# Kernel optimization log

Measured on AMD Instinct MI355X. Metric: run time of the kernel, lower is better.

## Reference

```python
import jax, jax.numpy as jnp
import numpy as np

N_NODES = 100000
N_EDGES = 1000000
IN_CH, HID_CH, N_CLS = 128, 64, 40


def setup_inputs() -> dict:
    key = jax.random.key(0)
    ks = jax.random.split(key, 8)
    x = jax.random.normal(ks[0], (N_NODES, IN_CH), dtype=jnp.float32)
    edge_index = jax.random.randint(ks[1], (2, N_EDGES), 0, N_NODES, dtype=jnp.int32)
    # Glorot-ish scaled weights (ARMAConv init_weight / root_weight, K=1 stack squeezed)
    w1_init = jax.random.normal(ks[2], (IN_CH, HID_CH), dtype=jnp.float32) / np.sqrt(IN_CH)
    w1_root = jax.random.normal(ks[3], (IN_CH, HID_CH), dtype=jnp.float32) / np.sqrt(IN_CH)
    b1 = jnp.zeros((HID_CH,), dtype=jnp.float32)
    w2_init = jax.random.normal(ks[4], (HID_CH, N_CLS), dtype=jnp.float32) / np.sqrt(HID_CH)
    w2_root = jax.random.normal(ks[5], (HID_CH, N_CLS), dtype=jnp.float32) / np.sqrt(HID_CH)
    b2 = jnp.zeros((N_CLS,), dtype=jnp.float32)
    return {"x": x, "edge_index": edge_index,
            "w1_init": w1_init, "w1_root": w1_root, "b1": b1,
            "w2_init": w2_init, "w2_root": w2_root, "b2": b2}


def _arma_layer(x, row, col, norm, w_init, w_root, bias):
    # ARMAConv, num_stacks=1, num_layers=1, shared_weights=True, eval mode (dropout=id):
    # out = relu( A_hat @ (x W_init) + x W_root + b ), mean over the single stack.
    h = x @ w_init                           # [N, F_out]
    msg = norm[:, None] * h[row]             # gather from source nodes, [E, F_out]
    agg = jax.ops.segment_sum(msg, col, num_segments=N_NODES)  # scatter-add at targets
    return jax.nn.relu(agg + x @ w_root + bias)


def reference(x, edge_index, w1_init, w1_root, b1, w2_init, w2_root, b2):
    row, col = edge_index[0], edge_index[1]
    # gcn_norm, add_self_loops=False: deg over targets, norm = d^-1/2[row] * d^-1/2[col]
    deg = jax.ops.segment_sum(jnp.ones((row.shape[0],), x.dtype), col, num_segments=N_NODES)
    dinv = jnp.where(deg > 0, jax.lax.rsqrt(jnp.maximum(deg, 1e-12)), jnp.zeros_like(deg))
    norm = dinv[row] * dinv[col]
    h = _arma_layer(x, row, col, norm, w1_init, w1_root, b1)
    h = jax.nn.relu(h)  # BiARMA relu; dropout identity in eval
    return _arma_layer(h, row, col, norm, w2_init, w2_root, b2)
```

## Files before the change

kernel.cpp:

```cpp
#include <hip/hip_runtime.h>

#define N_NODES 100000
#define N_EDGES 1000000
#define IN_CH 128
#define HID_CH 64
#define N_CLS 40

#define NBUCK 782
#define GEMM_GRID 1024

static inline int cdiv(int a, int b) { return (a + b - 1) / b; }

using bf16x8 = __attribute__((ext_vector_type(8))) short;
using f32x4  = __attribute__((ext_vector_type(4))) float;

__device__ __forceinline__ unsigned pack_bf2(float a, float b) {
    unsigned ua = __float_as_uint(a), ub = __float_as_uint(b);
    ua += 0x7fffu + ((ua >> 16) & 1u);
    ub += 0x7fffu + ((ub >> 16) & 1u);
    return (ua >> 16) | (ub & 0xffff0000u);
}
__device__ __forceinline__ unsigned short bf16_of(float a) {
    unsigned ua = __float_as_uint(a);
    ua += 0x7fffu + ((ua >> 16) & 1u);
    return (unsigned short)(ua >> 16);
}
__device__ __forceinline__ float bf_lo(unsigned u) { return __uint_as_float(u << 16); }
__device__ __forceinline__ float bf_hi(unsigned u) { return __uint_as_float(u & 0xffff0000u); }


__global__ __launch_bounds__(256)
void bucket_count_kernel(const int* __restrict__ cols, int* __restrict__ gcount, int E) {
    __shared__ int hist[NBUCK];
    for (int i = threadIdx.x; i < NBUCK; i += 256) hist[i] = 0;
    __syncthreads();
    int per = (E + gridDim.x - 1) / gridDim.x;
    int s = blockIdx.x * per;
    int e = min(E, s + per);
    for (int j = s + threadIdx.x; j < e; j += 256)
        atomicAdd(&hist[cols[j] >> 7], 1);
    __syncthreads();
    for (int i = threadIdx.x; i < NBUCK; i += 256)
        if (hist[i]) atomicAdd(&gcount[i], hist[i]);
}


__global__ __launch_bounds__(1024)
void scan_bucket_kernel(const int* __restrict__ gcount, int* __restrict__ boff,
                        int* __restrict__ gcursor, int* __restrict__ offsets) {
    __shared__ int part[1024];
    int t = threadIdx.x;
    part[t] = (t < NBUCK) ? gcount[t] : 0;
    __syncthreads();
    for (int off = 1; off < 1024; off <<= 1) {
        int v = (t >= off) ? part[t - off] : 0;
        __syncthreads();
        part[t] += v;
        __syncthreads();
    }
    int excl = (t > 0) ? part[t - 1] : 0;
    if (t < NBUCK) { boff[t] = excl; gcursor[t] = excl; }
    if (t == NBUCK) { boff[NBUCK] = excl; offsets[N_NODES] = excl; }
}


__global__ __launch_bounds__(256)
void bucket_scatter_kernel(const int* __restrict__ rows, const int* __restrict__ cols,
                           int* __restrict__ gcursor, int* __restrict__ pedge, int E) {
    __shared__ int cur[NBUCK];
    for (int i = threadIdx.x; i < NBUCK; i += 256) cur[i] = 0;
    __syncthreads();
    int per = (E + gridDim.x - 1) / gridDim.x;
    int s = blockIdx.x * per;
    int e = min(E, s + per);
    for (int j = s + threadIdx.x; j < e; j += 256)
        atomicAdd(&cur[cols[j] >> 7], 1);
    __syncthreads();
    for (int i = threadIdx.x; i < NBUCK; i += 256) {
        int h = cur[i];
        cur[i] = h ? atomicAdd(&gcursor[i], h) : 0;
    }
    __syncthreads();
    for (int j = s + threadIdx.x; j < e; j += 256) {
        int c = cols[j];
        int pos = atomicAdd(&cur[c >> 7], 1);
        pedge[pos] = (rows[j] << 7) | (c & 127);
    }
}


__global__ __launch_bounds__(256)
void bucket_sort_kernel(const int* __restrict__ boff, const int* __restrict__ pedge,
                        int* __restrict__ srow, int* __restrict__ offsets,
                        float* __restrict__ dinv) {
    __shared__ int cnt[128];
    __shared__ int scn[128];
    __shared__ int cur[128];
    int b = blockIdx.x, t = threadIdx.x;
    if (t < 128) cnt[t] = 0;
    __syncthreads();
    int e0 = boff[b], e1 = boff[b + 1];
    for (int j = e0 + t; j < e1; j += 256)
        atomicAdd(&cnt[pedge[j] & 127], 1);
    __syncthreads();
    if (t < 128) scn[t] = cnt[t];
    __syncthreads();
    for (int off = 1; off < 128; off <<= 1) {
        int v = 0;
        if (t < 128 && t >= off) v = scn[t - off];
        __syncthreads();
        if (t < 128) scn[t] += v;
        __syncthreads();
    }
    if (t < 128) {
        int excl = (t > 0) ? scn[t - 1] : 0;
        cur[t] = excl;
        int node = b * 128 + t;
        if (node < N_NODES) {
            offsets[node] = e0 + excl;
            dinv[node] = cnt[t] ? rsqrtf((float)cnt[t]) : 0.f;
        }
    }
    __syncthreads();
    for (int j = e0 + t; j < e1; j += 256) {
        int p = pedge[j];
        int pos = atomicAdd(&cur[p & 127], 1);
        srow[e0 + pos] = p >> 7;
    }
}


__global__ __launch_bounds__(256)
void wconv_kernel(const float* __restrict__ w1i, const float* __restrict__ w1r,
                  const float* __restrict__ w2i, const float* __restrict__ w2r,
                  unsigned* __restrict__ wtgA, unsigned* __restrict__ wtgB) {
    int id = blockIdx.x * 256 + threadIdx.x;
    if (id < 128 * 64) {
        int c = id >> 6, kp = id & 63;
        int k = kp * 2;
        const float* W = (c < 64) ? w1i : w1r;
        int cc = (c < 64) ? c : c - 64;
        float a = W[(size_t)k * 64 + cc];
        float b = W[(size_t)(k + 1) * 64 + cc];
        wtgA[c * 64 + kp] = pack_bf2(a, b);
    } else if (id < 128 * 64 + 80 * 32) {
        int j = id - 128 * 64;
        int c = j >> 5, kp = j & 31;
        int k = kp * 2;
        const float* W = (c < 40) ? w2i : w2r;
        int cc = (c < 40) ? c : c - 40;
        float a = W[(size_t)k * 40 + cc];
        float b = W[(size_t)(k + 1) * 40 + cc];
        wtgB[c * 32 + kp] = pack_bf2(a, b);
    }
}


template<int K, int C1, int C2>
__launch_bounds__(256, 4)
__global__ void gemm_persist_kernel(const float* __restrict__ X,
                                    const unsigned short* __restrict__ WT,
                                    const float* __restrict__ Bias,
                                    const float* __restrict__ dinv,
                                    unsigned short* __restrict__ Y1b,
                                    float* __restrict__ Y2, int N, int ntiles) {
    constexpr int CT = C1 + C2;
    constexpr int NT = CT / 16;
    constexpr int KS = K / 32;
    constexpr int KP = K / 2 + 4;
    static_assert(CT % 16 == 0 && K % 32 == 0, "shape");

    __shared__ unsigned wt[CT * KP];

    const int tid = threadIdx.x;
    const int wave = tid >> 6;
    const int lane = tid & 63;
    const int m = lane & 15;
    const int quad = lane >> 4;

    constexpr int WDW = CT * (K / 2);
    const unsigned* wtg = (const unsigned*)WT;
    for (int i = tid * 4; i < WDW; i += 256 * 4) {
        int c = i / (K / 2);
        int j = i - c * (K / 2);
        uint4 v = *reinterpret_cast<const uint4*>(wtg + i);
        *reinterpret_cast<uint4*>(&wt[c * KP + j]) = v;
    }
    __syncthreads();

    float biasv[NT];
#pragma unroll
    for (int t = 0; t < NT; ++t) {
        int c = t * 16 + m;
        biasv[t] = (c >= C1) ? Bias[c - C1] : 0.f;
    }

    for (int tile = blockIdx.x; tile < ntiles; tile += gridDim.x) {
        const int rowA = tile * 64 + wave * 16 + m;
        const bool va = (rowA < N);
        const float* xr = X + (size_t)rowA * K + quad * 8;

        union AFrag { uint4 u; bf16x8 v; } af[KS];
#pragma unroll
        for (int ks = 0; ks < KS; ++ks) {
            float4 v0 = make_float4(0.f, 0.f, 0.f, 0.f);
            float4 v1 = make_float4(0.f, 0.f, 0.f, 0.f);
            if (va) {
                v0 = *reinterpret_cast<const float4*>(xr + ks * 32);
                v1 = *reinterpret_cast<const float4*>(xr + ks * 32 + 4);
            }
            af[ks].u.x = pack_bf2(v0.x, v0.y);
            af[ks].u.y = pack_bf2(v0.z, v0.w);
            af[ks].u.z = pack_bf2(v1.x, v1.y);
            af[ks].u.w = pack_bf2(v1.z, v1.w);
        }

        f32x4 acc[NT];
#pragma unroll
        for (int t = 0; t < NT; ++t) acc[t] = (f32x4){0.f, 0.f, 0.f, 0.f};
#pragma unroll
        for (int ks = 0; ks < KS; ++ks) {
#pragma unroll
            for (int t = 0; t < NT; ++t) {
                bf16x8 b = *reinterpret_cast<const bf16x8*>(&wt[(t * 16 + m) * KP + ks * 16 + quad * 4]);
                acc[t] = __builtin_amdgcn_mfma_f32_16x16x32_bf16(af[ks].v, b, acc[t], 0, 0, 0);
            }
        }

        const int rbase = tile * 64 + wave * 16 + quad * 4;
        float dv[4];
#pragma unroll
        for (int reg = 0; reg < 4; ++reg)
            dv[reg] = (rbase + reg < N) ? dinv[rbase + reg] : 0.f;

#pragma unroll
        for (int t = 0; t < NT; ++t) {
            int c = t * 16 + m;
#pragma unroll
            for (int reg = 0; reg < 4; ++reg) {
                int r = rbase + reg;
                if (r >= N) continue;
                float v = acc[t][reg];
                if (c < C1) {
                    Y1b[(size_t)r * C1 + c] = bf16_of(v * dv[reg]);
                } else {
                    Y2[(size_t)r * C2 + (c - C1)] = v + biasv[t];
                }
            }
        }
    }
}


template<int K, int C1, int C2>
__launch_bounds__(256)
__global__ void gemm_mfma_fused_kernel(const float* __restrict__ X,
                                       const float* __restrict__ W1,
                                       const float* __restrict__ W2,
                                       const float* __restrict__ Bias,
                                       const float* __restrict__ dinv,
                                       unsigned short* __restrict__ Y1b,
                                       float* __restrict__ Y2, int N) {
    constexpr int CT = C1 + C2;
    constexpr int NT = CT / 16;
    constexpr int KS = K / 32;
    constexpr int KP = (K + 8) / 2;
    static_assert(CT % 16 == 0 && K % 32 == 0, "shape");
    static_assert(C1 % 4 == 0 && C2 % 4 == 0, "staging vec4");

    __shared__ unsigned xb[64 * KP];
    __shared__ unsigned wt[CT * KP];
    __shared__ float dloc[64];

    const int tid = threadIdx.x;
    const int wave = tid >> 6;
    const int lane = tid & 63;
    const int m = lane & 15;
    const int quad = lane >> 4;
    const int r0 = blockIdx.x * 64;

    if (tid < 64) {
        int gr = r0 + tid;
        dloc[tid] = (gr < N) ? dinv[gr] : 0.f;
    }

    constexpr int XIT = 64 * (K / 4);
    for (int i = tid; i < XIT; i += 256) {
        int rr = i / (K / 4);
        int k4 = i - rr * (K / 4);
        int gr = r0 + rr;
        float4 v = make_float4(0.f, 0.f, 0.f, 0.f);
        if (gr < N)
            v = *reinterpret_cast<const float4*>(&X[(size_t)gr * K + k4 * 4]);
        uint2 p;
        p.x = pack_bf2(v.x, v.y);
        p.y = pack_bf2(v.z, v.w);
        *reinterpret_cast<uint2*>(&xb[rr * KP + k4 * 2]) = p;
    }

    constexpr int WIT = (K / 2) * (CT / 4);
    for (int i = tid; i < WIT; i += 256) {
        int kp = i / (CT / 4);
        int c4 = i - kp * (CT / 4);
        int k = kp * 2;
        int c = c4 * 4;
        float4 va, vb;
        if (c < C1) {
            va = *reinterpret_cast<const float4*>(&W1[(size_t)k * C1 + c]);
            vb = *reinterpret_cast<const float4*>(&W1[(size_t)(k + 1) * C1 + c]);
        } else {
            va = *reinterpret_cast<const float4*>(&W2[(size_t)k * C2 + (c - C1)]);
            vb = *reinterpret_cast<const float4*>(&W2[(size_t)(k + 1) * C2 + (c - C1)]);
        }
        wt[(c + 0) * KP + kp] = pack_bf2(va.x, vb.x);
        wt[(c + 1) * KP + kp] = pack_bf2(va.y, vb.y);
        wt[(c + 2) * KP + kp] = pack_bf2(va.z, vb.z);
        wt[(c + 3) * KP + kp] = pack_bf2(va.w, vb.w);
    }
    __syncthreads();

    const int rowbase = wave * 16;
    f32x4 acc[NT];
#pragma unroll
    for (int t = 0; t < NT; ++t) acc[t] = (f32x4){0.f, 0.f, 0.f, 0.f};

#pragma unroll
    for (int ks = 0; ks < KS; ++ks) {
        bf16x8 a = *reinterpret_cast<const bf16x8*>(&xb[(rowbase + m) * KP + ks * 16 + quad * 4]);
#pragma unroll
        for (int t = 0; t < NT; ++t) {
            bf16x8 b = *reinterpret_cast<const bf16x8*>(&wt[(t * 16 + m) * KP + ks * 16 + quad * 4]);
            acc[t] = __builtin_amdgcn_mfma_f32_16x16x32_bf16(a, b, acc[t], 0, 0, 0);
        }
    }

#pragma unroll
    for (int t = 0; t < NT; ++t) {
        int c = t * 16 + m;
        float bias = (c >= C1) ? Bias[c - C1] : 0.f;
#pragma unroll
        for (int reg = 0; reg < 4; ++reg) {
            int rl = rowbase + quad * 4 + reg;
            int r = r0 + rl;
            if (r >= N) continue;
            float v = acc[t][reg];
            if (c < C1) {
                Y1b[(size_t)r * C1 + c] = bf16_of(v * dloc[rl]);
            } else {
                Y2[(size_t)r * C2 + (c - C1)] = v + bias;
            }
        }
    }
}


template<int C>
__launch_bounds__(256)
__global__ void pull_bf16_kernel(const int* __restrict__ offsets,
                                 const int* __restrict__ srow,
                                 const float* __restrict__ dinv,
                                 const unsigned* __restrict__ H,
                                 float* __restrict__ Y, int N) {
    constexpr int TPE = C / 4;
    constexpr int CH = C / 2;
    int gid = blockIdx.x * blockDim.x + threadIdx.x;
    int node = gid / TPE;
    int lane = gid - node * TPE;
    if (node >= N) return;

    int e0 = offsets[node];
    int e1 = offsets[node + 1];
    float dc = dinv[node];

    float4 acc = make_float4(0.f, 0.f, 0.f, 0.f);
    int j = e0;
    for (; j + 4 <= e1; j += 4) {
        int r0 = srow[j + 0];
        int r1 = srow[j + 1];
        int r2 = srow[j + 2];
        int r3 = srow[j + 3];
        uint2 u0 = *reinterpret_cast<const uint2*>(&H[(size_t)r0 * CH + lane * 2]);
        uint2 u1 = *reinterpret_cast<const uint2*>(&H[(size_t)r1 * CH + lane * 2]);
        uint2 u2 = *reinterpret_cast<const uint2*>(&H[(size_t)r2 * CH + lane * 2]);
        uint2 u3 = *reinterpret_cast<const uint2*>(&H[(size_t)r3 * CH + lane * 2]);
        acc.x += (bf_lo(u0.x) + bf_lo(u1.x)) + (bf_lo(u2.x) + bf_lo(u3.x));
        acc.y += (bf_hi(u0.x) + bf_hi(u1.x)) + (bf_hi(u2.x) + bf_hi(u3.x));
        acc.z += (bf_lo(u0.y) + bf_lo(u1.y)) + (bf_lo(u2.y) + bf_lo(u3.y));
        acc.w += (bf_hi(u0.y) + bf_hi(u1.y)) + (bf_hi(u2.y) + bf_hi(u3.y));
    }
    for (; j < e1; ++j) {
        int r = srow[j];
        uint2 u = *reinterpret_cast<const uint2*>(&H[(size_t)r * CH + lane * 2]);
        acc.x += bf_lo(u.x);
        acc.y += bf_hi(u.x);
        acc.z += bf_lo(u.y);
        acc.w += bf_hi(u.y);
    }

    float4* Y4 = reinterpret_cast<float4*>(Y);
    size_t yi = (size_t)node * TPE + lane;
    float4 y = Y4[yi];
    y.x = fmaxf(fmaf(dc, acc.x, y.x), 0.f);
    y.y = fmaxf(fmaf(dc, acc.y, y.y), 0.f);
    y.z = fmaxf(fmaf(dc, acc.z, y.z), 0.f);
    y.w = fmaxf(fmaf(dc, acc.w, y.w), 0.f);
    Y4[yi] = y;
}


extern "C" void kernel_launch(void* const* d_in, const int* in_sizes, int n_in,
                              void* d_out, int out_size, void* d_ws, size_t ws_size,
                              hipStream_t stream) {
    const float* x       = (const float*)d_in[0];
    const int*   eidx    = (const int*)d_in[1];
    const float* w1_init = (const float*)d_in[2];
    const float* w1_root = (const float*)d_in[3];
    const float* b1      = (const float*)d_in[4];
    const float* w2_init = (const float*)d_in[5];
    const float* w2_root = (const float*)d_in[6];
    const float* b2      = (const float*)d_in[7];
    float* out = (float*)d_out;

    const int* rows = eidx;
    const int* cols = eidx + N_EDGES;

    int* wsi = (int*)d_ws;
    int*      gcount  = wsi;
    int*      boff    = wsi + 784;
    int*      gcursor = wsi + 1572;
    float*    dinv    = (float*)(wsi + 2360);
    int*      offsets = wsi + 102360;
    int*      srow    = wsi + 202364;
    unsigned* h0b     = (unsigned*)(wsi + 1202364);
    int*      pedge   = wsi + 1202364;
    float*    agg1    = (float*)(wsi + 4402364);
    unsigned* h2b     = h0b;
    unsigned* wtgA    = (unsigned*)(wsi + 10802364);
    unsigned* wtgB    = wtgA + 8192;
    const size_t WS_NEEDED = 10813116ull * 4ull;

    hipMemsetAsync(gcount, 0, 784 * sizeof(int), stream);
    bucket_count_kernel<<<128, 256, 0, stream>>>(cols, gcount, N_EDGES);
    scan_bucket_kernel<<<1, 1024, 0, stream>>>(gcount, boff, gcursor, offsets);
    bucket_scatter_kernel<<<128, 256, 0, stream>>>(rows, cols, gcursor, pedge, N_EDGES);
    bucket_sort_kernel<<<NBUCK, 256, 0, stream>>>(boff, pedge, srow, offsets, dinv);

    const int NTILES = cdiv(N_NODES, 64);

    if (ws_size >= WS_NEEDED) {
        wconv_kernel<<<42, 256, 0, stream>>>(w1_init, w1_root, w2_init, w2_root, wtgA, wtgB);

        gemm_persist_kernel<IN_CH, HID_CH, HID_CH><<<GEMM_GRID, 256, 0, stream>>>(
            x, (const unsigned short*)wtgA, b1, dinv, (unsigned short*)h0b, agg1,
            N_NODES, NTILES);
        pull_bf16_kernel<HID_CH><<<cdiv(N_NODES * (HID_CH / 4), 256), 256, 0, stream>>>(
            offsets, srow, dinv, h0b, agg1, N_NODES);

        gemm_persist_kernel<HID_CH, N_CLS, N_CLS><<<GEMM_GRID, 256, 0, stream>>>(
            agg1, (const unsigned short*)wtgB, b2, dinv, (unsigned short*)h2b, out,
            N_NODES, NTILES);
        pull_bf16_kernel<N_CLS><<<cdiv(N_NODES * (N_CLS / 4), 256), 256, 0, stream>>>(
            offsets, srow, dinv, h2b, out, N_NODES);
    } else {
        gemm_mfma_fused_kernel<IN_CH, HID_CH, HID_CH><<<NTILES, 256, 0, stream>>>(
            x, w1_init, w1_root, b1, dinv, (unsigned short*)h0b, agg1, N_NODES);
        pull_bf16_kernel<HID_CH><<<cdiv(N_NODES * (HID_CH / 4), 256), 256, 0, stream>>>(
            offsets, srow, dinv, h0b, agg1, N_NODES);
        gemm_mfma_fused_kernel<HID_CH, N_CLS, N_CLS><<<NTILES, 256, 0, stream>>>(
            agg1, w2_init, w2_root, b2, dinv, (unsigned short*)h2b, out, N_NODES);
        pull_bf16_kernel<N_CLS><<<cdiv(N_NODES * (N_CLS / 4), 256), 256, 0, stream>>>(
            offsets, srow, dinv, h2b, out, N_NODES);
    }
}
```

Before: 282.0 us.

## Fuse weight conversion into bucket count and stage GEMM epilogue through LDS

Weight bf16 packing moves into extra blocks of the bucket-count kernel, which removes one launch. The persistent GEMM with weights staged in LDS becomes a one-tile-per-block kernel that reads B fragments straight from global (L2-resident) memory. Its epilogue now writes results into per-wave LDS buffers and then stores coalesced 16-byte rows, replacing scattered 2- and 4-byte stores. The cost is more blocks launched and uncached global weight loads in the MFMA loop.

```diff
diff --git a/kernel.cpp b/kernel.cpp
--- a/kernel.cpp
+++ b/kernel.cpp
@@ -7,7 +7,6 @@
 #define N_CLS 40
 
 #define NBUCK 782
-#define GEMM_GRID 1024
 
 static inline int cdiv(int a, int b) { return (a + b - 1) / b; }
 
@@ -30,11 +29,37 @@
 
 
 __global__ __launch_bounds__(256)
-void bucket_count_kernel(const int* __restrict__ cols, int* __restrict__ gcount, int E) {
+void bucket_count_wconv_kernel(const int* __restrict__ cols, int* __restrict__ gcount, int E,
+                               const float* __restrict__ w1i, const float* __restrict__ w1r,
+                               const float* __restrict__ w2i, const float* __restrict__ w2r,
+                               unsigned* __restrict__ wtgA, unsigned* __restrict__ wtgB) {
+    if (blockIdx.x >= 128) {
+        if (wtgA == nullptr) return;
+        int id = (blockIdx.x - 128) * 256 + threadIdx.x;
+        if (id < 128 * 64) {
+            int c = id >> 6, kp = id & 63;
+            int k = kp * 2;
+            const float* W = (c < 64) ? w1i : w1r;
+            int cc = (c < 64) ? c : c - 64;
+            float a = W[(size_t)k * 64 + cc];
+            float b = W[(size_t)(k + 1) * 64 + cc];
+            wtgA[c * 64 + kp] = pack_bf2(a, b);
+        } else if (id < 128 * 64 + 80 * 32) {
+            int j = id - 128 * 64;
+            int c = j >> 5, kp = j & 31;
+            int k = kp * 2;
+            const float* W = (c < 40) ? w2i : w2r;
+            int cc = (c < 40) ? c : c - 40;
+            float a = W[(size_t)k * 40 + cc];
+            float b = W[(size_t)(k + 1) * 40 + cc];
+            wtgB[c * 32 + kp] = pack_bf2(a, b);
+        }
+        return;
+    }
     __shared__ int hist[NBUCK];
     for (int i = threadIdx.x; i < NBUCK; i += 256) hist[i] = 0;
     __syncthreads();
-    int per = (E + gridDim.x - 1) / gridDim.x;
+    int per = (E + 127) / 128;
     int s = blockIdx.x * per;
     int e = min(E, s + per);
     for (int j = s + threadIdx.x; j < e; j += 256)
@@ -130,122 +155,108 @@
 }
 
 
-__global__ __launch_bounds__(256)
-void wconv_kernel(const float* __restrict__ w1i, const float* __restrict__ w1r,
-                  const float* __restrict__ w2i, const float* __restrict__ w2r,
-                  unsigned* __restrict__ wtgA, unsigned* __restrict__ wtgB) {
-    int id = blockIdx.x * 256 + threadIdx.x;
-    if (id < 128 * 64) {
-        int c = id >> 6, kp = id & 63;
-        int k = kp * 2;
-        const float* W = (c < 64) ? w1i : w1r;
-        int cc = (c < 64) ? c : c - 64;
-        float a = W[(size_t)k * 64 + cc];
-        float b = W[(size_t)(k + 1) * 64 + cc];
-        wtgA[c * 64 + kp] = pack_bf2(a, b);
-    } else if (id < 128 * 64 + 80 * 32) {
-        int j = id - 128 * 64;
-        int c = j >> 5, kp = j & 31;
-        int k = kp * 2;
-        const float* W = (c < 40) ? w2i : w2r;
-        int cc = (c < 40) ? c : c - 40;
-        float a = W[(size_t)k * 40 + cc];
-        float b = W[(size_t)(k + 1) * 40 + cc];
-        wtgB[c * 32 + kp] = pack_bf2(a, b);
-    }
-}
-
-
 template<int K, int C1, int C2>
-__launch_bounds__(256, 4)
-__global__ void gemm_persist_kernel(const float* __restrict__ X,
-                                    const unsigned short* __restrict__ WT,
-                                    const float* __restrict__ Bias,
-                                    const float* __restrict__ dinv,
-                                    unsigned short* __restrict__ Y1b,
-                                    float* __restrict__ Y2, int N, int ntiles) {
+__launch_bounds__(256, 6)
+__global__ void gemm_fat_kernel(const float* __restrict__ X,
+                                const unsigned short* __restrict__ WT,
+                                const float* __restrict__ Bias,
+                                const float* __restrict__ dinv,
+                                unsigned short* __restrict__ Y1b,
+                                float* __restrict__ Y2, int N) {
     constexpr int CT = C1 + C2;
     constexpr int NT = CT / 16;
     constexpr int KS = K / 32;
-    constexpr int KP = K / 2 + 4;
-    static_assert(CT % 16 == 0 && K % 32 == 0, "shape");
-
-    __shared__ unsigned wt[CT * KP];
+    constexpr int S16 = 72;
+    constexpr int SF  = 68;
+    static_assert(CT % 16 == 0 && K % 32 == 0 && C1 % 8 == 0 && C2 % 4 == 0, "shape");
+
+    __shared__ unsigned short eb16[4 * 16 * S16];
+    __shared__ float          ebf [4 * 16 * SF];
 
     const int tid = threadIdx.x;
     const int wave = tid >> 6;
     const int lane = tid & 63;
     const int m = lane & 15;
     const int quad = lane >> 4;
-
-    constexpr int WDW = CT * (K / 2);
-    const unsigned* wtg = (const unsigned*)WT;
-    for (int i = tid * 4; i < WDW; i += 256 * 4) {
-        int c = i / (K / 2);
-        int j = i - c * (K / 2);
-        uint4 v = *reinterpret_cast<const uint4*>(wtg + i);
-        *reinterpret_cast<uint4*>(&wt[c * KP + j]) = v;
-    }
-    __syncthreads();
-
-    float biasv[NT];
+    const int r0 = blockIdx.x * 64;
+
+    const int rowA = r0 + wave * 16 + m;
+    const bool va = (rowA < N);
+    const float* xr = X + (size_t)rowA * K + quad * 8;
+
+    union AFrag { uint4 u; bf16x8 v; } af[KS];
+#pragma unroll
+    for (int ks = 0; ks < KS; ++ks) {
+        float4 v0 = make_float4(0.f, 0.f, 0.f, 0.f);
+        float4 v1 = make_float4(0.f, 0.f, 0.f, 0.f);
+        if (va) {
+            v0 = *reinterpret_cast<const float4*>(xr + ks * 32);
+            v1 = *reinterpret_cast<const float4*>(xr + ks * 32 + 4);
+        }
+        af[ks].u.x = pack_bf2(v0.x, v0.y);
+        af[ks].u.y = pack_bf2(v0.z, v0.w);
+        af[ks].u.z = pack_bf2(v1.x, v1.y);
+        af[ks].u.w = pack_bf2(v1.z, v1.w);
+    }
+
+    f32x4 acc[NT];
+#pragma unroll
+    for (int t = 0; t < NT; ++t) acc[t] = (f32x4){0.f, 0.f, 0.f, 0.f};
+#pragma unroll
+    for (int ks = 0; ks < KS; ++ks) {
+#pragma unroll
+        for (int t = 0; t < NT; ++t) {
+            bf16x8 b = *reinterpret_cast<const bf16x8*>(&WT[(size_t)(t * 16 + m) * K + ks * 32 + quad * 8]);
+            acc[t] = __builtin_amdgcn_mfma_f32_16x16x32_bf16(af[ks].v, b, acc[t], 0, 0, 0);
+        }
+    }
+
+    const int rbase0 = r0 + wave * 16;
+    const int rbase = rbase0 + quad * 4;
+    float dv[4];
+#pragma unroll
+    for (int reg = 0; reg < 4; ++reg)
+        dv[reg] = (rbase + reg < N) ? dinv[rbase + reg] : 0.f;
+
+    unsigned short* e16 = &eb16[wave * 16 * S16];
+    float* ef = &ebf[wave * 16 * SF];
 #pragma unroll
     for (int t = 0; t < NT; ++t) {
         int c = t * 16 + m;
-        biasv[t] = (c >= C1) ? Bias[c - C1] : 0.f;
-    }
-
-    for (int tile = blockIdx.x; tile < ntiles; tile += gridDim.x) {
-        const int rowA = tile * 64 + wave * 16 + m;
-        const bool va = (rowA < N);
-        const float* xr = X + (size_t)rowA * K + quad * 8;
-
-        union AFrag { uint4 u; bf16x8 v; } af[KS];
-#pragma unroll
-        for (int ks = 0; ks < KS; ++ks) {
-            float4 v0 = make_float4(0.f, 0.f, 0.f, 0.f);
-            float4 v1 = make_float4(0.f, 0.f, 0.f, 0.f);
-            if (va) {
-                v0 = *reinterpret_cast<const float4*>(xr + ks * 32);
-                v1 = *reinterpret_cast<const float4*>(xr + ks * 32 + 4);
+        if (c < C1) {
+#pragma unroll
+            for (int reg = 0; reg < 4; ++reg)
+                e16[(quad * 4 + reg) * S16 + c] = bf16_of(acc[t][reg] * dv[reg]);
+        } else {
+            float b = Bias[c - C1];
+#pragma unroll
+            for (int reg = 0; reg < 4; ++reg)
+                ef[(quad * 4 + reg) * SF + (c - C1)] = acc[t][reg] + b;
+        }
+    }
+    __syncthreads();
+
+    constexpr int SEG1 = C1 / 8;
+    for (int it = 0; it < (16 * SEG1 + 63) / 64; ++it) {
+        int task = lane + it * 64;
+        if (task < 16 * SEG1) {
+            int row = task / SEG1, seg = task - row * SEG1;
+            int gr = rbase0 + row;
+            if (gr < N) {
+                uint4 v = *reinterpret_cast<const uint4*>(&eb16[(wave * 16 + row) * S16 + seg * 8]);
+                *reinterpret_cast<uint4*>(&Y1b[(size_t)gr * C1 + seg * 8]) = v;
             }
-            af[ks].u.x = pack_bf2(v0.x, v0.y);
-            af[ks].u.y = pack_bf2(v0.z, v0.w);
-            af[ks].u.z = pack_bf2(v1.x, v1.y);
-            af[ks].u.w = pack_bf2(v1.z, v1.w);
-        }
-
-        f32x4 acc[NT];
-#pragma unroll
-        for (int t = 0; t < NT; ++t) acc[t] = (f32x4){0.f, 0.f, 0.f, 0.f};
-#pragma unroll
-        for (int ks = 0; ks < KS; ++ks) {
-#pragma unroll
-            for (int t = 0; t < NT; ++t) {
-                bf16x8 b = *reinterpret_cast<const bf16x8*>(&wt[(t * 16 + m) * KP + ks * 16 + quad * 4]);
-                acc[t] = __builtin_amdgcn_mfma_f32_16x16x32_bf16(af[ks].v, b, acc[t], 0, 0, 0);
-            }
-        }
-
-        const int rbase = tile * 64 + wave * 16 + quad * 4;
-        float dv[4];
-#pragma unroll
-        for (int reg = 0; reg < 4; ++reg)
-            dv[reg] = (rbase + reg < N) ? dinv[rbase + reg] : 0.f;
-
-#pragma unroll
-        for (int t = 0; t < NT; ++t) {
-            int c = t * 16 + m;
-#pragma unroll
-            for (int reg = 0; reg < 4; ++reg) {
-                int r = rbase + reg;
-                if (r >= N) continue;
-                float v = acc[t][reg];
-                if (c < C1) {
-                    Y1b[(size_t)r * C1 + c] = bf16_of(v * dv[reg]);
-                } else {
-                    Y2[(size_t)r * C2 + (c - C1)] = v + biasv[t];
-                }
+        }
+    }
+    constexpr int SEG2 = C2 / 4;
+    for (int it = 0; it < (16 * SEG2 + 63) / 64; ++it) {
+        int task = lane + it * 64;
+        if (task < 16 * SEG2) {
+            int row = task / SEG2, seg = task - row * SEG2;
+            int gr = rbase0 + row;
+            if (gr < N) {
+                float4 v = *reinterpret_cast<const float4*>(&ebf[(wave * 16 + row) * SF + seg * 4]);
+                *reinterpret_cast<float4*>(&Y2[(size_t)gr * C2 + seg * 4]) = v;
             }
         }
     }
@@ -439,26 +450,26 @@
     unsigned* wtgB    = wtgA + 8192;
     const size_t WS_NEEDED = 10813116ull * 4ull;
 
+    const bool have_wt = (ws_size >= WS_NEEDED);
+
     hipMemsetAsync(gcount, 0, 784 * sizeof(int), stream);
-    bucket_count_kernel<<<128, 256, 0, stream>>>(cols, gcount, N_EDGES);
+    bucket_count_wconv_kernel<<<170, 256, 0, stream>>>(
+        cols, gcount, N_EDGES, w1_init, w1_root, w2_init, w2_root,
+        have_wt ? wtgA : nullptr, have_wt ? wtgB : nullptr);
     scan_bucket_kernel<<<1, 1024, 0, stream>>>(gcount, boff, gcursor, offsets);
     bucket_scatter_kernel<<<128, 256, 0, stream>>>(rows, cols, gcursor, pedge, N_EDGES);
     bucket_sort_kernel<<<NBUCK, 256, 0, stream>>>(boff, pedge, srow, offsets, dinv);
 
     const int NTILES = cdiv(N_NODES, 64);
 
-    if (ws_size >= WS_NEEDED) {
-        wconv_kernel<<<42, 256, 0, stream>>>(w1_init, w1_root, w2_init, w2_root, wtgA, wtgB);
-
-        gemm_persist_kernel<IN_CH, HID_CH, HID_CH><<<GEMM_GRID, 256, 0, stream>>>(
-            x, (const unsigned short*)wtgA, b1, dinv, (unsigned short*)h0b, agg1,
-            N_NODES, NTILES);
+    if (have_wt) {
+        gemm_fat_kernel<IN_CH, HID_CH, HID_CH><<<NTILES, 256, 0, stream>>>(
+            x, (const unsigned short*)wtgA, b1, dinv, (unsigned short*)h0b, agg1, N_NODES);
         pull_bf16_kernel<HID_CH><<<cdiv(N_NODES * (HID_CH / 4), 256), 256, 0, stream>>>(
             offsets, srow, dinv, h0b, agg1, N_NODES);
 
-        gemm_persist_kernel<HID_CH, N_CLS, N_CLS><<<GEMM_GRID, 256, 0, stream>>>(
-            agg1, (const unsigned short*)wtgB, b2, dinv, (unsigned short*)h2b, out,
-            N_NODES, NTILES);
+        gemm_fat_kernel<HID_CH, N_CLS, N_CLS><<<NTILES, 256, 0, stream>>>(
+            agg1, (const unsigned short*)wtgB, b2, dinv, (unsigned short*)h2b, out, N_NODES);
         pull_bf16_kernel<N_CLS><<<cdiv(N_NODES * (N_CLS / 4), 256), 256, 0, stream>>>(
             offsets, srow, dinv, h2b, out, N_NODES);
     } else {
```

Result: faster. 263.7 us (-6.5%).
